# Performance work log

Hardware: AMD Instinct MI355X
Metric: run time of the kernel (lower is better)

Reference implementation:

```python
import jax, jax.numpy as jnp
import numpy as np

C, N, E = 256, 256, 2048          # subgraphs, nodes/subgraph, edges/subgraph
F_IN, NHID, DDI = 128, 128, 256
K1, K2, K3 = 128, 64, 32          # top-k sizes for pooling_ratio=0.5
P, B = 16, 16                     # DAG hierarchy: P parents x B leaf children
GN = C + P + 1                    # global DAG nodes (leaves + parents + root)
GE = 8192                         # global pos/neg edge count


def setup_inputs():
    key = jax.random.key(0)
    ks = jax.random.split(key, 16)
    inp = {
        "x": jax.random.normal(ks[0], (C, N, F_IN), jnp.float32),
        "edge_index": jax.random.randint(ks[1], (C, 2, E), 0, N),
        "edge_weight": jax.random.uniform(ks[2], (C, E), dtype=jnp.float32),
        "global_edge_index": jax.random.randint(ks[3], (2, GE), 0, GN),
        "neg_edge_index": jax.random.randint(ks[4], (2, GE), 0, GN),
    }
    names = [("W1", F_IN, NHID), ("Wp1", NHID, 1), ("W2", NHID, NHID),
             ("Wp2", NHID, 1), ("W3", NHID, NHID), ("Wp3", NHID, 1),
             ("Wg", 6 * NHID, DDI), ("Wl1", DDI, DDI), ("Wl2", DDI, DDI)]
    for i, (nm, fi, fo) in enumerate(names):
        inp[nm] = jax.random.normal(ks[5 + i], (fi, fo), jnp.float32) / np.sqrt(fi)
        inp["b" + nm[1:]] = jnp.zeros((fo,), jnp.float32)
    return inp


def gcn(x, ei, ew, W, b):
    """PyG GCNConv with self-loops: D^-1/2 (A+I) D^-1/2 X W + b."""
    n = x.shape[0]
    h = x @ W
    row, col = ei[0], ei[1]
    deg = 1.0 + jax.ops.segment_sum(ew, col, num_segments=n)
    dis = jax.lax.rsqrt(deg)
    norm = dis[row] * ew * dis[col]                       # [E]
    agg = jax.ops.segment_sum(norm[:, None] * h[row], col, num_segments=n)
    return agg + h / deg[:, None] + b


def sag_pool(x, ei, ew, Ws, bs, k):
    """SAGPooling: GCN score, per-graph top-k, gate by tanh(score), edge filter."""
    n = x.shape[0]
    score = gcn(x, ei, ew, Ws, bs)[:, 0]
    vals, perm = jax.lax.top_k(score, k)
    x_new = x[perm] * jnp.tanh(vals)[:, None]
    newid = jnp.full((n,), -1, jnp.int32).at[perm].set(jnp.arange(k, dtype=jnp.int32))
    r, c = newid[ei[0]], newid[ei[1]]
    keep = (r >= 0) & (c >= 0)
    ei_new = jnp.where(keep, jnp.stack([r, c]), 0)        # dropped edges -> node 0
    ew_new = jnp.where(keep, ew, 0.0)                     # with zero weight
    return x_new, ei_new, ew_new


def _subgraph(x, ei, ew, W1, b1, Wp1, bp1, W2, b2, Wp2, bp2, W3, b3, Wp3, bp3):
    x = jax.nn.relu(gcn(x, ei, ew, W1, b1))
    x, ei, ew = sag_pool(x, ei, ew, Wp1, bp1, K1)
    x1 = jnp.concatenate([x.max(0), x.mean(0)])           # gmp||gap, batch all-zero
    x = jax.nn.relu(gcn(x, ei, ew, W2, b2))
    x, ei, ew = sag_pool(x, ei, ew, Wp2, bp2, K2)
    x2 = jnp.concatenate([x.max(0), x.mean(0)])
    x = jax.nn.relu(gcn(x, ei, ew, W3, b3))
    x, ei, ew = sag_pool(x, ei, ew, Wp3, bp3, K3)
    x3 = jnp.concatenate([x.max(0), x.mean(0)])
    return jnp.concatenate([x1, x2, x3])                  # [6*NHID]


def reference(x, edge_index, edge_weight, global_edge_index, neg_edge_index,
              W1, b1, Wp1, bp1, W2, b2, Wp2, bp2, W3, b3, Wp3, bp3,
              Wg, bg, Wl1, bl1, Wl2, bl2):
    # per-class subgraph pipeline, vmapped over the C subgraphs
    leaf = jax.vmap(_subgraph, in_axes=(0, 0, 0) + (None,) * 12)(
        x, edge_index, edge_weight,
        W1, b1, Wp1, bp1, W2, b2, Wp2, bp2, W3, b3, Wp3, bp3)   # [C, 6*NHID]
    # Get_Fs: mean-aggregate children features up the DAG (fixed 2-level + root)
    parent = leaf.reshape(P, B, -1).mean(axis=1)                # [P, 6*NHID]
    root = parent.mean(axis=0, keepdims=True)                   # [1, 6*NHID]
    gfeat = jnp.concatenate([leaf, parent, root], axis=0)       # [GN, 6*NHID]
    # global GCN (unit edge weights)
    gx = jax.nn.relu(gcn(gfeat, global_edge_index,
                         jnp.ones((GE,), gfeat.dtype), Wg, bg)) # [GN, DDI]
    class_embedding = gx[:C]
    # feature_split + lin1/lin2 + dot-product scores
    pos_s = gx[global_edge_index[0]] @ Wl1 + bl1
    pos_t = gx[global_edge_index[1]] @ Wl2 + bl2
    neg_s = gx[neg_edge_index[0]] @ Wl1 + bl1
    neg_t = gx[neg_edge_index[1]] @ Wl2 + bl2
    pos = jnp.sum(pos_s * pos_t, axis=1)
    neg = jnp.sum(neg_s * neg_t, axis=1)
    # BCEWithLogits: targets 1 for pos, 0 for neg
    loss = jnp.mean(jax.nn.softplus(-pos)) + jnp.mean(jax.nn.softplus(neg))
    return class_embedding, loss
```

## Files before the change

### kernel.cpp

```cpp
#include <hip/hip_runtime.h>
#include <math.h>

#define NT 1024
#define EDGES 2048
#define SENT 0xFFFF

struct SmemA {
  float xbuf[256 * 128];
  unsigned short rc[EDGES];
  float ewl[EDGES];
  unsigned short csr_row[EDGES];
  float csr_coef[EDGES];
  float degs[256];
  float diss[256];
  int   csr_off[257];
  int   csr_cnt[256];
  float hsv[256];
  float scorev[256];
  float vals[128];
  short perm[128];
  signed char newid[256];
};

__device__ __forceinline__ float4* xvec(float* xb, int row, int c4) {
  return reinterpret_cast<float4*>(xb + (row << 7) + ((c4 ^ (row & 7)) << 2));
}
__device__ __forceinline__ int xidx(int row, int col) {
  return (row << 7) + ((((col >> 2) ^ (row & 7)) << 2) | (col & 3));
}

template<int NN, int K, bool FIRST, bool REMAP>
__device__ __forceinline__ void run_stage(
    SmemA& sm,
    const float* __restrict__ xg,
    const int* __restrict__ eic,
    const float* __restrict__ ewc,
    const float* __restrict__ W,
    const float* __restrict__ b,
    const float* __restrict__ Wp,
    const float* __restrict__ bp,
    float* __restrict__ leaf_out)
{
  constexpr int NPT  = NN / 64;
  constexpr int Q    = NN / 64;
  constexpr int SEG  = NT / NN;
  constexpr int LEN  = NN / SEG;
  constexpr int LOG  = (NN == 256) ? 8 : (NN == 128 ? 7 : 6);
  const int tid  = threadIdx.x;
  const int lane = tid & 63;
  const int fbase = __builtin_amdgcn_readfirstlane((tid >> 6) << 3);
  const int c4b   = fbase >> 2;

  if (tid < NN) { sm.degs[tid] = 1.0f; sm.csr_cnt[tid] = 0; }
  __syncthreads();

  if (FIRST) {
    const float4* xg4 = reinterpret_cast<const float4*>(xg);
    for (int i = tid; i < 256 * 32; i += NT) {
      const float4 v = xg4[i];
      *xvec(sm.xbuf, i >> 5, i & 31) = v;
    }
    for (int e = tid; e < EDGES; e += NT) {
      const int row = eic[e], col = eic[EDGES + e];
      const float w = ewc[e];
      sm.rc[e]  = (unsigned short)((row << 8) | col);
      sm.ewl[e] = w;
      atomicAdd(&sm.degs[col], w);
      atomicAdd(&sm.csr_cnt[col], 1);
    }
  } else {
    for (int e = tid; e < EDGES; e += NT) {
      const unsigned short r = sm.rc[e];
      if (r != SENT) {
        atomicAdd(&sm.degs[r & 255], sm.ewl[e]);
        atomicAdd(&sm.csr_cnt[r & 255], 1);
      }
    }
  }
  __syncthreads();

  if (tid < NN) sm.diss[tid] = rsqrtf(sm.degs[tid]);
  if (tid < 64) {
    int c[Q], pre[Q];
    int tot = 0;
#pragma unroll
    for (int i = 0; i < Q; i++) { c[i] = sm.csr_cnt[tid * Q + i]; pre[i] = tot; tot += c[i]; }
    int inc = tot;
#pragma unroll
    for (int d = 1; d < 64; d <<= 1) {
      const int o = __shfl_up(inc, d, 64);
      if (tid >= d) inc += o;
    }
    const int base = inc - tot;
    if (tid == 0) sm.csr_off[0] = 0;
#pragma unroll
    for (int i = 0; i < Q; i++) {
      sm.csr_off[tid * Q + i + 1] = base + pre[i] + c[i];
      sm.csr_cnt[tid * Q + i] = 0;
    }
  }
  __syncthreads();

  for (int e = tid; e < EDGES; e += NT) {
    const unsigned short r = sm.rc[e];
    if (FIRST || r != SENT) {
      const int row = r >> 8, col = r & 255;
      const int p = atomicAdd(&sm.csr_cnt[col], 1);
      const int s = sm.csr_off[col] + p;
      sm.csr_row[s]  = (unsigned short)row;
      sm.csr_coef[s] = sm.diss[row] * sm.ewl[e];
    }
  }
  __syncthreads();

  float acc[NPT][8];
#pragma unroll
  for (int i = 0; i < NPT; i++)
#pragma unroll
    for (int j = 0; j < 8; j++) acc[i][j] = 0.0f;

#pragma unroll 4
  for (int k4 = 0; k4 < 32; k4++) {
    float4 xv[NPT];
#pragma unroll
    for (int i = 0; i < NPT; i++) xv[i] = *xvec(sm.xbuf, lane + (i << 6), k4);
#pragma unroll
    for (int kk = 0; kk < 4; kk++) {
      const float* wr = W + (((k4 << 2) + kk) << 7) + fbase;
      const float4 wa = *reinterpret_cast<const float4*>(wr);
      const float4 wb = *reinterpret_cast<const float4*>(wr + 4);
      const float wv[8] = {wa.x, wa.y, wa.z, wa.w, wb.x, wb.y, wb.z, wb.w};
      const float xk[1] = {0};
      (void)xk;
#pragma unroll
      for (int i = 0; i < NPT; i++) {
        const float xs = (kk == 0) ? xv[i].x : (kk == 1) ? xv[i].y : (kk == 2) ? xv[i].z : xv[i].w;
#pragma unroll
        for (int j = 0; j < 8; j++) acc[i][j] = fmaf(xs, wv[j], acc[i][j]);
      }
    }
  }
  __syncthreads();

#pragma unroll
  for (int i = 0; i < NPT; i++) {
    const int v = lane + (i << 6);
    *xvec(sm.xbuf, v, c4b)     = make_float4(acc[i][0], acc[i][1], acc[i][2], acc[i][3]);
    *xvec(sm.xbuf, v, c4b + 1) = make_float4(acc[i][4], acc[i][5], acc[i][6], acc[i][7]);
  }
  __syncthreads();

  float agg[NPT][8];
#pragma unroll
  for (int i = 0; i < NPT; i++) {
    const int v = lane + (i << 6);
    const int beg = sm.csr_off[v], end = sm.csr_off[v + 1];
#pragma unroll
    for (int j = 0; j < 8; j++) agg[i][j] = 0.0f;
    int r_nxt = 0; float c_nxt = 0.0f;
    if (beg < end) { r_nxt = sm.csr_row[beg]; c_nxt = sm.csr_coef[beg]; }
    for (int s = beg; s < end; ++s) {
      const int r = r_nxt; const float cf = c_nxt;
      if (s + 1 < end) { r_nxt = sm.csr_row[s + 1]; c_nxt = sm.csr_coef[s + 1]; }
      const float4 lo = *xvec(sm.xbuf, r, c4b);
      const float4 hi = *xvec(sm.xbuf, r, c4b + 1);
      agg[i][0] = fmaf(cf, lo.x, agg[i][0]);
      agg[i][1] = fmaf(cf, lo.y, agg[i][1]);
      agg[i][2] = fmaf(cf, lo.z, agg[i][2]);
      agg[i][3] = fmaf(cf, lo.w, agg[i][3]);
      agg[i][4] = fmaf(cf, hi.x, agg[i][4]);
      agg[i][5] = fmaf(cf, hi.y, agg[i][5]);
      agg[i][6] = fmaf(cf, hi.z, agg[i][6]);
      agg[i][7] = fmaf(cf, hi.w, agg[i][7]);
    }
  }
  if (tid < NN) sm.hsv[tid] = 0.0f;
  __syncthreads();

  {
    const float4 ba = *reinterpret_cast<const float4*>(b + fbase);
    const float4 bb = *reinterpret_cast<const float4*>(b + fbase + 4);
    const float bv[8] = {ba.x, ba.y, ba.z, ba.w, bb.x, bb.y, bb.z, bb.w};
#pragma unroll
    for (int i = 0; i < NPT; i++) {
      const int v = lane + (i << 6);
      const float dv = sm.diss[v];
      const float invd = 1.0f / sm.degs[v];
#pragma unroll
      for (int j = 0; j < 8; j++)
        acc[i][j] = fmaxf(fmaf(agg[i][j], dv, fmaf(acc[i][j], invd, bv[j])), 0.0f);
      *xvec(sm.xbuf, v, c4b)     = make_float4(acc[i][0], acc[i][1], acc[i][2], acc[i][3]);
      *xvec(sm.xbuf, v, c4b + 1) = make_float4(acc[i][4], acc[i][5], acc[i][6], acc[i][7]);
    }
    const float4 wa = *reinterpret_cast<const float4*>(Wp + fbase);
    const float4 wb = *reinterpret_cast<const float4*>(Wp + fbase + 4);
    const float wv[8] = {wa.x, wa.y, wa.z, wa.w, wb.x, wb.y, wb.z, wb.w};
#pragma unroll
    for (int i = 0; i < NPT; i++) {
      float part = 0.0f;
#pragma unroll
      for (int j = 0; j < 8; j++) part = fmaf(acc[i][j], wv[j], part);
      atomicAdd(&sm.hsv[lane + (i << 6)], part);
    }
  }
  __syncthreads();

  if (tid < NN) {
    const int v = tid;
    const int beg = sm.csr_off[v], end = sm.csr_off[v + 1];
    float s = 0.0f;
    for (int e2 = beg; e2 < end; e2++)
      s = fmaf(sm.csr_coef[e2], sm.hsv[sm.csr_row[e2]], s);
    sm.scorev[v] = s * sm.diss[v] + sm.hsv[v] / sm.degs[v] + bp[0];
    sm.csr_cnt[v] = 0;
  }
  __syncthreads();

  {
    const int node = tid & (NN - 1);
    const int seg  = tid >> LOG;
    const float sv = sm.scorev[node];
    int part = 0;
    const int u0 = seg * LEN;
#pragma unroll 4
    for (int u = u0; u < u0 + LEN; u++) {
      const float su = sm.scorev[u];
      part += (su > sv) || (su == sv && u < node);
    }
    if (part) atomicAdd(&sm.csr_cnt[node], part);
  }
  __syncthreads();
  if (tid < NN) {
    const int rank = sm.csr_cnt[tid];
    if (rank < K) { sm.perm[rank] = (short)tid; sm.vals[rank] = sm.scorev[tid]; sm.newid[tid] = (signed char)rank; }
    else sm.newid[tid] = -1;
  }
  __syncthreads();

  {
    constexpr int TPR = NT / K;
    constexpr int C4  = 32 / TPR;
    const int drow = tid / TPR;
    const int cc   = (tid % TPR) * C4;
    const int src  = sm.perm[drow];
    const float g  = tanhf(sm.vals[drow]);
    float4 tmp[C4];
#pragma unroll
    for (int j = 0; j < C4; j++) tmp[j] = *xvec(sm.xbuf, src, cc + j);
    __syncthreads();
#pragma unroll
    for (int j = 0; j < C4; j++) {
      tmp[j].x *= g; tmp[j].y *= g; tmp[j].z *= g; tmp[j].w *= g;
      *xvec(sm.xbuf, drow, cc + j) = tmp[j];
    }
  }
  __syncthreads();

  if (tid < 128) {
    float mx = -INFINITY, sv = 0.0f;
    for (int i = 0; i < K; i++) {
      const float v = sm.xbuf[xidx(i, tid)];
      mx = fmaxf(mx, v); sv += v;
    }
    leaf_out[tid] = mx;
    leaf_out[128 + tid] = sv * (1.0f / K);
  }
  if (REMAP) {
    for (int e = tid; e < EDGES; e += NT) {
      const unsigned short r = sm.rc[e];
      if (FIRST || r != SENT) {
        const int r2 = sm.newid[r >> 8];
        const int c2 = sm.newid[r & 255];
        sm.rc[e] = (r2 < 0 || c2 < 0) ? (unsigned short)SENT
                                      : (unsigned short)((r2 << 8) | c2);
      }
    }
  }
  __syncthreads();
}

__global__ __launch_bounds__(NT)
void stageA_kernel(const float* __restrict__ x0,
                   const int* __restrict__ ei, const float* __restrict__ ew,
                   const float* __restrict__ W1, const float* __restrict__ b1,
                   const float* __restrict__ Wp1, const float* __restrict__ bp1,
                   const float* __restrict__ W2, const float* __restrict__ b2,
                   const float* __restrict__ Wp2, const float* __restrict__ bp2,
                   const float* __restrict__ W3, const float* __restrict__ b3,
                   const float* __restrict__ Wp3, const float* __restrict__ bp3,
                   float* __restrict__ gfeat)
{
  __shared__ SmemA sm;
  const int c = blockIdx.x;
  const int* eic = ei + (size_t)c * 2 * EDGES;
  const float* ewc = ew + (size_t)c * EDGES;
  const float* xgc = x0 + (size_t)c * 256 * 128;
  float* leaf = gfeat + (size_t)c * 768;
  run_stage<256, 128, true,  true >(sm, xgc, eic, ewc, W1, b1, Wp1, bp1, leaf + 0);
  run_stage<128,  64, false, true >(sm, nullptr, nullptr, nullptr, W2, b2, Wp2, bp2, leaf + 256);
  run_stage< 64,  32, false, false>(sm, nullptr, nullptr, nullptr, W3, b3, Wp3, bp3, leaf + 512);
}

__global__ __launch_bounds__(256)
void gmm_k(const float* __restrict__ gfeat, const float* __restrict__ Wg,
           float* __restrict__ hG, const int* __restrict__ gei,
           float* __restrict__ degG, float* __restrict__ lacc,
           int* __restrict__ lctr) {
  const int v = blockIdx.x, f = threadIdx.x;
  if (v == 273) {
    __shared__ int cnt[273];
    for (int i = f; i < 273; i += 256) cnt[i] = 0;
    __syncthreads();
    for (int e = f; e < 8192; e += 256) atomicAdd(&cnt[gei[8192 + e]], 1);
    __syncthreads();
    for (int i = f; i < 273; i += 256) degG[i] = 1.0f + (float)cnt[i];
    if (f == 0) { *lacc = 0.0f; *lctr = 0; }
    return;
  }
  __shared__ float gf[768];
  if (v < 256) {
    for (int k = f; k < 768; k += 256) gf[k] = gfeat[(size_t)v * 768 + k];
  } else if (v < 272) {
    const int p = v - 256;
    for (int k = f; k < 768; k += 256) {
      float s = 0.0f;
      for (int b2 = 0; b2 < 16; b2++) s += gfeat[(size_t)(p * 16 + b2) * 768 + k];
      gf[k] = s * (1.0f / 16.0f);
    }
  } else {
    for (int k = f; k < 768; k += 256) {
      float s = 0.0f;
      for (int i = 0; i < 256; i++) s += gfeat[(size_t)i * 768 + k];
      gf[k] = s * (1.0f / 256.0f);
    }
  }
  __syncthreads();
  float a = 0.0f;
#pragma unroll 8
  for (int k = 0; k < 768; k++) a = fmaf(gf[k], Wg[(size_t)k * 256 + f], a);
  hG[(size_t)v * 256 + f] = a;
}

__global__ __launch_bounds__(256)
void gaggemb_k(const float* __restrict__ hG, const float* __restrict__ degG,
               const int* __restrict__ gei, const float* __restrict__ bg,
               const float* __restrict__ Wl1, const float* __restrict__ bl1,
               const float* __restrict__ Wl2, const float* __restrict__ bl2,
               float* __restrict__ out_ce, float* __restrict__ A,
               float* __restrict__ B) {
  __shared__ int lrows[8192];
  __shared__ int lcnt;
  __shared__ float gxr[256];
  const int v = blockIdx.x, tid = threadIdx.x;
  if (tid == 0) lcnt = 0;
  __syncthreads();
  for (int e = tid; e < 8192; e += 256)
    if (gei[8192 + e] == v) { int p = atomicAdd(&lcnt, 1); lrows[p] = gei[e]; }
  __syncthreads();
  const int n = lcnt;
  float a = 0.0f;
  for (int i = 0; i < n; i++) {
    const int r = lrows[i];
    a += rsqrtf(degG[r]) * hG[(size_t)r * 256 + tid];
  }
  float val = a * rsqrtf(degG[v]) + hG[(size_t)v * 256 + tid] / degG[v] + bg[tid];
  val = fmaxf(val, 0.0f);
  gxr[tid] = val;
  if (v < 256) out_ce[(size_t)v * 256 + tid] = val;
  __syncthreads();
  float aa = bl1[tid], bb = bl2[tid];
#pragma unroll 4
  for (int k = 0; k < 256; k++) {
    const float gv = gxr[k];
    aa = fmaf(gv, Wl1[(size_t)k * 256 + tid], aa);
    bb = fmaf(gv, Wl2[(size_t)k * 256 + tid], bb);
  }
  A[(size_t)v * 256 + tid] = aa;
  B[(size_t)v * 256 + tid] = bb;
}

__global__ void loss_k(const float* __restrict__ A, const float* __restrict__ B,
                       const int* __restrict__ gei, const int* __restrict__ nei,
                       float* __restrict__ acc, int* __restrict__ lctr,
                       float* __restrict__ out) {
  const int gw = (blockIdx.x * blockDim.x + threadIdx.x) >> 6;
  const int lane = threadIdx.x & 63;
  float lsum = 0.0f;
  for (int idx = gw; idx < 16384; idx += 512) {
    const bool ispos = idx < 8192;
    const int e = ispos ? idx : idx - 8192;
    const int* ia = ispos ? gei : nei;
    const int s = ia[e], t = ia[8192 + e];
    float p = 0.0f;
#pragma unroll
    for (int j = 0; j < 4; j++)
      p += A[(size_t)s * 256 + lane + 64 * j] * B[(size_t)t * 256 + lane + 64 * j];
#pragma unroll
    for (int off = 32; off; off >>= 1) p += __shfl_xor(p, off, 64);
    const float z = ispos ? -p : p;
    lsum += fmaxf(z, 0.0f) + log1pf(expf(-fabsf(z)));
  }
  if (lane == 0) atomicAdd(acc, lsum);
  __syncthreads();
  if (threadIdx.x == 0) {
    __threadfence();
    const int old = atomicAdd(lctr, 1);
    if (old == (int)gridDim.x - 1) {
      const float tot = atomicAdd(acc, 0.0f);
      out[65536] = tot * (1.0f / 8192.0f);
    }
  }
}

extern "C" void kernel_launch(void* const* d_in, const int* in_sizes, int n_in,
                              void* d_out, int out_size, void* d_ws, size_t ws_size,
                              hipStream_t stream) {
  const float* x   = (const float*)d_in[0];
  const int*   ei  = (const int*)d_in[1];
  const float* ew  = (const float*)d_in[2];
  const int*   gei = (const int*)d_in[3];
  const int*   nei = (const int*)d_in[4];
  const float* W1  = (const float*)d_in[5];
  const float* b1  = (const float*)d_in[6];
  const float* Wp1 = (const float*)d_in[7];
  const float* bp1 = (const float*)d_in[8];
  const float* W2  = (const float*)d_in[9];
  const float* b2  = (const float*)d_in[10];
  const float* Wp2 = (const float*)d_in[11];
  const float* bp2 = (const float*)d_in[12];
  const float* W3  = (const float*)d_in[13];
  const float* b3  = (const float*)d_in[14];
  const float* Wp3 = (const float*)d_in[15];
  const float* bp3 = (const float*)d_in[16];
  const float* Wg  = (const float*)d_in[17];
  const float* bg  = (const float*)d_in[18];
  const float* Wl1 = (const float*)d_in[19];
  const float* bl1 = (const float*)d_in[20];
  const float* Wl2 = (const float*)d_in[21];
  const float* bl2 = (const float*)d_in[22];

  float* ws    = (float*)d_ws;
  float* gfeat = ws;
  float* hG    = gfeat + 256 * 768;
  float* degG  = hG + 273 * 256;
  float* Aemb  = degG + 288;
  float* Bemb  = Aemb + 273 * 256;
  float* lacc  = Bemb + 273 * 256;
  int*   lctr  = (int*)(lacc + 1);
  float* out   = (float*)d_out;

  stageA_kernel<<<256, NT, 0, stream>>>(x, ei, ew, W1, b1, Wp1, bp1,
                                        W2, b2, Wp2, bp2, W3, b3, Wp3, bp3, gfeat);
  gmm_k<<<274, 256, 0, stream>>>(gfeat, Wg, hG, gei, degG, lacc, lctr);
  gaggemb_k<<<273, 256, 0, stream>>>(hG, degG, gei, bg, Wl1, bl1, Wl2, bl2,
                                     out, Aemb, Bemb);
  loss_k<<<128, 256, 0, stream>>>(Aemb, Bemb, gei, nei, lacc, lctr, out);
}
```

Measured before the change: 223.6 us.

## Fuse leaf Wg projection into stage kernel and use linearity for parent/root

Each subgraph block now multiplies its own leaf features by Wg right after pooling. A small prep kernel handles the parent rows by averaging leaf features, and the root row is built by accumulating parent projections, relying on mean-then-matmul linearity. Degree and CSR counting for later pooling stages moves into the edge-remap pass, which removes one full edge sweep per stage. The global aggregation caps each node's neighbour list at 512 to shrink shared memory, and unrolls its accumulations. Risks: atomic float ordering changes rounding, and the 512 neighbour cap silently drops edges for any node with more incoming edges.

```diff
diff --git a/kernel.cpp b/kernel.cpp
--- a/kernel.cpp
+++ b/kernel.cpp
@@ -39,7 +39,8 @@
     const float* __restrict__ b,
     const float* __restrict__ Wp,
     const float* __restrict__ bp,
-    float* __restrict__ leaf_out)
+    float* __restrict__ leaf_out,
+    float& lmax, float& lmean)
 {
   constexpr int NPT  = NN / 64;
   constexpr int Q    = NN / 64;
@@ -51,10 +52,9 @@
   const int fbase = __builtin_amdgcn_readfirstlane((tid >> 6) << 3);
   const int c4b   = fbase >> 2;
 
-  if (tid < NN) { sm.degs[tid] = 1.0f; sm.csr_cnt[tid] = 0; }
-  __syncthreads();
-
   if (FIRST) {
+    if (tid < NN) { sm.degs[tid] = 1.0f; sm.csr_cnt[tid] = 0; }
+    __syncthreads();
     const float4* xg4 = reinterpret_cast<const float4*>(xg);
     for (int i = tid; i < 256 * 32; i += NT) {
       const float4 v = xg4[i];
@@ -68,16 +68,8 @@
       atomicAdd(&sm.degs[col], w);
       atomicAdd(&sm.csr_cnt[col], 1);
     }
-  } else {
-    for (int e = tid; e < EDGES; e += NT) {
-      const unsigned short r = sm.rc[e];
-      if (r != SENT) {
-        atomicAdd(&sm.degs[r & 255], sm.ewl[e]);
-        atomicAdd(&sm.csr_cnt[r & 255], 1);
-      }
-    }
-  }
-  __syncthreads();
+    __syncthreads();
+  }
 
   if (tid < NN) sm.diss[tid] = rsqrtf(sm.degs[tid]);
   if (tid < 64) {
@@ -130,8 +122,6 @@
       const float4 wa = *reinterpret_cast<const float4*>(wr);
       const float4 wb = *reinterpret_cast<const float4*>(wr + 4);
       const float wv[8] = {wa.x, wa.y, wa.z, wa.w, wb.x, wb.y, wb.z, wb.w};
-      const float xk[1] = {0};
-      (void)xk;
 #pragma unroll
       for (int i = 0; i < NPT; i++) {
         const float xs = (kk == 0) ? xv[i].x : (kk == 1) ? xv[i].y : (kk == 2) ? xv[i].z : xv[i].w;
@@ -234,6 +224,7 @@
     const int rank = sm.csr_cnt[tid];
     if (rank < K) { sm.perm[rank] = (short)tid; sm.vals[rank] = sm.scorev[tid]; sm.newid[tid] = (signed char)rank; }
     else sm.newid[tid] = -1;
+    if (tid < K) { sm.degs[tid] = 1.0f; sm.csr_cnt[tid] = 0; }
   }
   __syncthreads();
 
@@ -262,8 +253,10 @@
       const float v = sm.xbuf[xidx(i, tid)];
       mx = fmaxf(mx, v); sv += v;
     }
+    lmax = mx;
+    lmean = sv * (1.0f / K);
     leaf_out[tid] = mx;
-    leaf_out[128 + tid] = sv * (1.0f / K);
+    leaf_out[128 + tid] = lmean;
   }
   if (REMAP) {
     for (int e = tid; e < EDGES; e += NT) {
@@ -271,8 +264,12 @@
       if (FIRST || r != SENT) {
         const int r2 = sm.newid[r >> 8];
         const int c2 = sm.newid[r & 255];
-        sm.rc[e] = (r2 < 0 || c2 < 0) ? (unsigned short)SENT
-                                      : (unsigned short)((r2 << 8) | c2);
+        if (r2 < 0 || c2 < 0) sm.rc[e] = SENT;
+        else {
+          sm.rc[e] = (unsigned short)((r2 << 8) | c2);
+          atomicAdd(&sm.degs[c2], sm.ewl[e]);
+          atomicAdd(&sm.csr_cnt[c2], 1);
+        }
       }
     }
   }
@@ -288,57 +285,99 @@
                    const float* __restrict__ Wp2, const float* __restrict__ bp2,
                    const float* __restrict__ W3, const float* __restrict__ b3,
                    const float* __restrict__ Wp3, const float* __restrict__ bp3,
-                   float* __restrict__ gfeat)
+                   const float* __restrict__ Wg,
+                   float* __restrict__ gfeat, float* __restrict__ hG)
 {
   __shared__ SmemA sm;
   const int c = blockIdx.x;
+  const int tid = threadIdx.x;
+  if (c == 0 && tid < 256) hG[(size_t)272 * 256 + tid] = 0.0f;
   const int* eic = ei + (size_t)c * 2 * EDGES;
   const float* ewc = ew + (size_t)c * EDGES;
   const float* xgc = x0 + (size_t)c * 256 * 128;
   float* leaf = gfeat + (size_t)c * 768;
-  run_stage<256, 128, true,  true >(sm, xgc, eic, ewc, W1, b1, Wp1, bp1, leaf + 0);
-  run_stage<128,  64, false, true >(sm, nullptr, nullptr, nullptr, W2, b2, Wp2, bp2, leaf + 256);
-  run_stage< 64,  32, false, false>(sm, nullptr, nullptr, nullptr, W3, b3, Wp3, bp3, leaf + 512);
-}
-
-__global__ __launch_bounds__(256)
-void gmm_k(const float* __restrict__ gfeat, const float* __restrict__ Wg,
-           float* __restrict__ hG, const int* __restrict__ gei,
-           float* __restrict__ degG, float* __restrict__ lacc,
-           int* __restrict__ lctr) {
-  const int v = blockIdx.x, f = threadIdx.x;
-  if (v == 273) {
+  float l0 = 0.f, l1 = 0.f, l2 = 0.f, l3 = 0.f, l4 = 0.f, l5 = 0.f;
+  run_stage<256, 128, true,  true >(sm, xgc, eic, ewc, W1, b1, Wp1, bp1, leaf + 0,   l0, l1);
+  run_stage<128,  64, false, true >(sm, nullptr, nullptr, nullptr, W2, b2, Wp2, bp2, leaf + 256, l2, l3);
+  run_stage< 64,  32, false, false>(sm, nullptr, nullptr, nullptr, W3, b3, Wp3, bp3, leaf + 512, l4, l5);
+
+  float* leafbuf = sm.csr_coef;
+  float* hGacc   = sm.degs;
+  if (tid < 256) {
+    if (tid < 128) {
+      leafbuf[tid]       = l0; leafbuf[128 + tid] = l1;
+      leafbuf[256 + tid] = l2; leafbuf[384 + tid] = l3;
+      leafbuf[512 + tid] = l4; leafbuf[640 + tid] = l5;
+    }
+    hGacc[tid] = 0.0f;
+  }
+  __syncthreads();
+  {
+    const int f = tid & 255, q = tid >> 8;
+    const float* wgq = Wg + (size_t)(q * 192) * 256 + f;
+    const float* lb  = leafbuf + q * 192;
+    float p0 = 0.f, p1 = 0.f, p2 = 0.f, p3 = 0.f;
+    for (int i = 0; i < 192; i += 4) {
+      p0 = fmaf(lb[i],     wgq[(size_t)i * 256],      p0);
+      p1 = fmaf(lb[i + 1], wgq[(size_t)(i + 1) * 256], p1);
+      p2 = fmaf(lb[i + 2], wgq[(size_t)(i + 2) * 256], p2);
+      p3 = fmaf(lb[i + 3], wgq[(size_t)(i + 3) * 256], p3);
+    }
+    atomicAdd(&hGacc[f], (p0 + p1) + (p2 + p3));
+  }
+  __syncthreads();
+  if (tid < 256) hG[(size_t)c * 256 + tid] = hGacc[tid];
+}
+
+__global__ __launch_bounds__(NT)
+void prep_k(const float* __restrict__ gfeat, const float* __restrict__ Wg,
+            float* __restrict__ hG, const int* __restrict__ gei,
+            float* __restrict__ degG, float* __restrict__ lacc,
+            int* __restrict__ lctr) {
+  const int tid = threadIdx.x;
+  if (blockIdx.x == 16) {
     __shared__ int cnt[273];
-    for (int i = f; i < 273; i += 256) cnt[i] = 0;
+    for (int i = tid; i < 273; i += NT) cnt[i] = 0;
     __syncthreads();
-    for (int e = f; e < 8192; e += 256) atomicAdd(&cnt[gei[8192 + e]], 1);
+    for (int e = tid; e < 8192; e += NT) atomicAdd(&cnt[gei[8192 + e]], 1);
     __syncthreads();
-    for (int i = f; i < 273; i += 256) degG[i] = 1.0f + (float)cnt[i];
-    if (f == 0) { *lacc = 0.0f; *lctr = 0; }
+    for (int i = tid; i < 273; i += NT) degG[i] = 1.0f + (float)cnt[i];
+    if (tid == 0) { *lacc = 0.0f; *lctr = 0; }
     return;
   }
-  __shared__ float gf[768];
-  if (v < 256) {
-    for (int k = f; k < 768; k += 256) gf[k] = gfeat[(size_t)v * 768 + k];
-  } else if (v < 272) {
-    const int p = v - 256;
-    for (int k = f; k < 768; k += 256) {
-      float s = 0.0f;
-      for (int b2 = 0; b2 < 16; b2++) s += gfeat[(size_t)(p * 16 + b2) * 768 + k];
-      gf[k] = s * (1.0f / 16.0f);
-    }
-  } else {
-    for (int k = f; k < 768; k += 256) {
-      float s = 0.0f;
-      for (int i = 0; i < 256; i++) s += gfeat[(size_t)i * 768 + k];
-      gf[k] = s * (1.0f / 256.0f);
-    }
-  }
-  __syncthreads();
-  float a = 0.0f;
-#pragma unroll 8
-  for (int k = 0; k < 768; k++) a = fmaf(gf[k], Wg[(size_t)k * 256 + f], a);
-  hG[(size_t)v * 256 + f] = a;
+  const int p = blockIdx.x;
+  __shared__ float prow[768];
+  __shared__ float hGacc[256];
+  for (int k = tid; k < 768; k += NT) {
+    float s0 = 0.f, s1 = 0.f;
+#pragma unroll
+    for (int b2 = 0; b2 < 16; b2 += 2) {
+      s0 += gfeat[(size_t)(p * 16 + b2) * 768 + k];
+      s1 += gfeat[(size_t)(p * 16 + b2 + 1) * 768 + k];
+    }
+    prow[k] = (s0 + s1) * (1.0f / 16.0f);
+  }
+  if (tid < 256) hGacc[tid] = 0.0f;
+  __syncthreads();
+  {
+    const int f = tid & 255, q = tid >> 8;
+    const float* wgq = Wg + (size_t)(q * 192) * 256 + f;
+    const float* lb  = prow + q * 192;
+    float p0 = 0.f, p1 = 0.f, p2 = 0.f, p3 = 0.f;
+    for (int i = 0; i < 192; i += 4) {
+      p0 = fmaf(lb[i],     wgq[(size_t)i * 256],      p0);
+      p1 = fmaf(lb[i + 1], wgq[(size_t)(i + 1) * 256], p1);
+      p2 = fmaf(lb[i + 2], wgq[(size_t)(i + 2) * 256], p2);
+      p3 = fmaf(lb[i + 3], wgq[(size_t)(i + 3) * 256], p3);
+    }
+    atomicAdd(&hGacc[f], (p0 + p1) + (p2 + p3));
+  }
+  __syncthreads();
+  if (tid < 256) {
+    const float hv = hGacc[tid];
+    hG[(size_t)(256 + p) * 256 + tid] = hv;
+    atomicAdd(&hG[(size_t)272 * 256 + tid], hv * (1.0f / 16.0f));
+  }
 }
 
 __global__ __launch_bounds__(256)
@@ -348,41 +387,60 @@
                const float* __restrict__ Wl2, const float* __restrict__ bl2,
                float* __restrict__ out_ce, float* __restrict__ A,
                float* __restrict__ B) {
-  __shared__ int lrows[8192];
-  __shared__ int lcnt;
+  __shared__ int   lrows[512];
+  __shared__ float lcoef[512];
   __shared__ float gxr[256];
+  __shared__ int   lcnt;
   const int v = blockIdx.x, tid = threadIdx.x;
   if (tid == 0) lcnt = 0;
   __syncthreads();
   for (int e = tid; e < 8192; e += 256)
-    if (gei[8192 + e] == v) { int p = atomicAdd(&lcnt, 1); lrows[p] = gei[e]; }
-  __syncthreads();
-  const int n = lcnt;
-  float a = 0.0f;
-  for (int i = 0; i < n; i++) {
-    const int r = lrows[i];
-    a += rsqrtf(degG[r]) * hG[(size_t)r * 256 + tid];
-  }
-  float val = a * rsqrtf(degG[v]) + hG[(size_t)v * 256 + tid] / degG[v] + bg[tid];
+    if (gei[8192 + e] == v) {
+      const int p = atomicAdd(&lcnt, 1);
+      if (p < 512) lrows[p] = gei[e];
+    }
+  __syncthreads();
+  const int n = min(lcnt, 512);
+  for (int i = tid; i < n; i += 256) lcoef[i] = rsqrtf(degG[lrows[i]]);
+  __syncthreads();
+  float a0 = 0.f, a1 = 0.f, a2 = 0.f, a3 = 0.f;
+  int i = 0;
+  for (; i + 4 <= n; i += 4) {
+    a0 = fmaf(lcoef[i],     hG[(size_t)lrows[i]     * 256 + tid], a0);
+    a1 = fmaf(lcoef[i + 1], hG[(size_t)lrows[i + 1] * 256 + tid], a1);
+    a2 = fmaf(lcoef[i + 2], hG[(size_t)lrows[i + 2] * 256 + tid], a2);
+    a3 = fmaf(lcoef[i + 3], hG[(size_t)lrows[i + 3] * 256 + tid], a3);
+  }
+  for (; i < n; i++) a0 = fmaf(lcoef[i], hG[(size_t)lrows[i] * 256 + tid], a0);
+  const float dg = degG[v];
+  float val = ((a0 + a1) + (a2 + a3)) * rsqrtf(dg)
+            + hG[(size_t)v * 256 + tid] / dg + bg[tid];
   val = fmaxf(val, 0.0f);
   gxr[tid] = val;
   if (v < 256) out_ce[(size_t)v * 256 + tid] = val;
   __syncthreads();
-  float aa = bl1[tid], bb = bl2[tid];
-#pragma unroll 4
-  for (int k = 0; k < 256; k++) {
-    const float gv = gxr[k];
-    aa = fmaf(gv, Wl1[(size_t)k * 256 + tid], aa);
-    bb = fmaf(gv, Wl2[(size_t)k * 256 + tid], bb);
-  }
-  A[(size_t)v * 256 + tid] = aa;
-  B[(size_t)v * 256 + tid] = bb;
-}
-
-__global__ void loss_k(const float* __restrict__ A, const float* __restrict__ B,
-                       const int* __restrict__ gei, const int* __restrict__ nei,
-                       float* __restrict__ acc, int* __restrict__ lctr,
-                       float* __restrict__ out) {
+  float aa0 = bl1[tid], aa1 = 0.f, aa2 = 0.f, aa3 = 0.f;
+  float bb0 = bl2[tid], bb1 = 0.f, bb2 = 0.f, bb3 = 0.f;
+  for (int k = 0; k < 256; k += 4) {
+    const float g0 = gxr[k], g1 = gxr[k + 1], g2 = gxr[k + 2], g3 = gxr[k + 3];
+    aa0 = fmaf(g0, Wl1[(size_t)k * 256 + tid],       aa0);
+    aa1 = fmaf(g1, Wl1[(size_t)(k + 1) * 256 + tid], aa1);
+    aa2 = fmaf(g2, Wl1[(size_t)(k + 2) * 256 + tid], aa2);
+    aa3 = fmaf(g3, Wl1[(size_t)(k + 3) * 256 + tid], aa3);
+    bb0 = fmaf(g0, Wl2[(size_t)k * 256 + tid],       bb0);
+    bb1 = fmaf(g1, Wl2[(size_t)(k + 1) * 256 + tid], bb1);
+    bb2 = fmaf(g2, Wl2[(size_t)(k + 2) * 256 + tid], bb2);
+    bb3 = fmaf(g3, Wl2[(size_t)(k + 3) * 256 + tid], bb3);
+  }
+  A[(size_t)v * 256 + tid] = (aa0 + aa1) + (aa2 + aa3);
+  B[(size_t)v * 256 + tid] = (bb0 + bb1) + (bb2 + bb3);
+}
+
+__global__ __launch_bounds__(256)
+void loss_k(const float* __restrict__ A, const float* __restrict__ B,
+            const int* __restrict__ gei, const int* __restrict__ nei,
+            float* __restrict__ acc, int* __restrict__ lctr,
+            float* __restrict__ out) {
   const int gw = (blockIdx.x * blockDim.x + threadIdx.x) >> 6;
   const int lane = threadIdx.x & 63;
   float lsum = 0.0f;
@@ -450,8 +508,9 @@
   float* out   = (float*)d_out;
 
   stageA_kernel<<<256, NT, 0, stream>>>(x, ei, ew, W1, b1, Wp1, bp1,
-                                        W2, b2, Wp2, bp2, W3, b3, Wp3, bp3, gfeat);
-  gmm_k<<<274, 256, 0, stream>>>(gfeat, Wg, hG, gei, degG, lacc, lctr);
+                                        W2, b2, Wp2, bp2, W3, b3, Wp3, bp3,
+                                        Wg, gfeat, hG);
+  prep_k<<<17, NT, 0, stream>>>(gfeat, Wg, hG, gei, degG, lacc, lctr);
   gaggemb_k<<<273, 256, 0, stream>>>(hG, degG, gei, bg, Wl1, bl1, Wl2, bl2,
                                      out, Aemb, Bemb);
   loss_k<<<128, 256, 0, stream>>>(Aemb, Bemb, gei, nei, lacc, lctr, out);
```

After: 182.5 us. 1.23x faster.
